# Kernel optimization log

Measured on AMD Instinct MI355X. Metric: run time of the kernel, lower is better.

Reference implementation:

```python
import jax, jax.numpy as jnp
import numpy as np

B, S, H, N_HEAD = 2, 2048, 1024, 16
NEG = float(-(2 ** 32) + 1)  # -4294967295.0, the module's padding value
EPS = 1e-08


def setup_inputs() -> dict:
    key = jax.random.key(0)
    ks = jax.random.split(key, 11)
    sc = 0.02
    return {
        "queries": jax.random.normal(ks[0], (B, S, H), dtype=jnp.float32),
        "keys": jax.random.normal(ks[1], (B, S, H), dtype=jnp.float32),
        "values": jax.random.normal(ks[2], (B, S, H), dtype=jnp.float32),
        "Wq": jax.random.normal(ks[3], (H, H), dtype=jnp.float32) * sc,
        "bq": jax.random.normal(ks[4], (H,), dtype=jnp.float32) * sc,
        "Wk": jax.random.normal(ks[5], (H, H), dtype=jnp.float32) * sc,
        "bk": jax.random.normal(ks[6], (H,), dtype=jnp.float32) * sc,
        "Wv": jax.random.normal(ks[7], (H, H), dtype=jnp.float32) * sc,
        "bv": jax.random.normal(ks[8], (H,), dtype=jnp.float32) * sc,
        "Wo": jax.random.normal(ks[9], (H, H), dtype=jnp.float32) * sc,
        "bo": jax.random.normal(ks[10], (H,), dtype=jnp.float32) * sc,
    }


def reference(queries, keys, values, Wq, bq, Wk, bk, Wv, bv, Wo, bo):
    n = N_HEAD
    Bb, Sq, Hh = queries.shape
    Sk = keys.shape[1]
    d = Hh // n

    # Linear + ReLU projections
    Q = jax.nn.relu(queries @ Wq + bq)  # [B,Sq,H]
    K = jax.nn.relu(keys @ Wk + bk)     # [B,Sk,H]
    V = jax.nn.relu(values @ Wv + bv)   # [B,Sk,H]

    # chunk(dim=2) + cat(dim=0) == head-major split: [n,B,S,d]
    Q_ = Q.reshape(Bb, Sq, n, d).transpose(2, 0, 1, 3)
    K_ = K.reshape(Bb, Sk, n, d).transpose(2, 0, 1, 3)
    V_ = V.reshape(Bb, Sk, n, d).transpose(2, 0, 1, 3)

    # key padding mask from full (pre-chunk) K: [B,Sk]
    key_masks = jnp.sign(jnp.abs(jnp.sum(K, axis=-1)))

    # scores: [n,B,Sq,Sk], scaled by sqrt(per-head dim)
    scores = jnp.einsum("hbqd,hbkd->hbqk", Q_, K_) / (d ** 0.5)

    # multiplicative padding-mask selection -> equivalent where()
    scores = jnp.where(key_masks[None, :, None, :] == 0.0, NEG, scores)

    # causal tril mask (masked=True)
    tril = jnp.tril(jnp.ones((Sq, Sk), dtype=scores.dtype))
    scores = jnp.where(tril[None, None] == 0.0, NEG, scores)

    attn = jax.nn.softmax(scores, axis=-1)
    out = jnp.einsum("hbqk,hbkd->hbqd", attn, V_)  # [n,B,Sq,d]

    # cat chunks back along feature dim: [B,Sq,H]
    out = out.transpose(1, 2, 0, 3).reshape(Bb, Sq, Hh)

    out = jax.nn.relu(out @ Wo + bo)
    # sublayer connection (dropout treated as identity for determinism)
    out = queries + out

    # layer norm with torch-style unbiased std, gamma=1, beta=0
    mean = out.mean(axis=-1, keepdims=True)
    std = jnp.std(out, axis=-1, ddof=1, keepdims=True)
    return (out - mean) / (std + EPS)
```

## Files before the change

### kernel.cpp

```cpp
#include <hip/hip_runtime.h>
#include <math.h>

typedef __bf16 bf16;
typedef __attribute__((ext_vector_type(8))) __bf16 bf16x8;
typedef __attribute__((ext_vector_type(4))) __bf16 bf16x4;
typedef __attribute__((ext_vector_type(4))) float f32x4;

typedef __attribute__((address_space(1))) unsigned int glb_u32;
typedef __attribute__((address_space(3))) unsigned int lds_u32;

#define NEGV (-4294967295.0f)
#define SCL2 0.18033688011112042f

__device__ __forceinline__ void async_cp16(const void* g, void* l) {
  __builtin_amdgcn_global_load_lds((glb_u32*)g, (lds_u32*)l, 16, 0, 0);
}

template <int CTRL>
__device__ __forceinline__ float dppf(float x) {
  return __builtin_bit_cast(float,
      __builtin_amdgcn_mov_dpp(__builtin_bit_cast(int, x), CTRL, 0xF, 0xF, true));
}
__device__ __forceinline__ float dpp_max16(float x) {
  x = fmaxf(x, dppf<0xB1>(x));
  x = fmaxf(x, dppf<0x4E>(x));
  x = fmaxf(x, dppf<0x141>(x));
  x = fmaxf(x, dppf<0x140>(x));
  return x;
}
__device__ __forceinline__ float dpp_sum16(float x) {
  x += dppf<0xB1>(x);
  x += dppf<0x4E>(x);
  x += dppf<0x141>(x);
  x += dppf<0x140>(x);
  return x;
}

__global__ __launch_bounds__(256) void cvt3_kernel(
    const float* __restrict__ q, const float* __restrict__ k,
    const float* __restrict__ v, short* xq, short* xk, short* xv) {
  const int bid = blockIdx.x;
  const int which = bid >> 12;
  const int i = (bid & 4095) * 256 + threadIdx.x;
  const float* src = which == 0 ? q : (which == 1 ? k : v);
  short* dst = which == 0 ? xq : (which == 1 ? xk : xv);
  float4 vv = ((const float4*)src)[i];
  bf16x4 o;
  o[0] = (bf16)vv.x; o[1] = (bf16)vv.y; o[2] = (bf16)vv.z; o[3] = (bf16)vv.w;
  ((bf16x4*)dst)[i] = o;
}

__global__ __launch_bounds__(256) void wt_kernel(
    const float* __restrict__ W0, const float* __restrict__ W1,
    const float* __restrict__ W2, const float* __restrict__ W3,
    short* T0, short* T1, short* T2, short* T3) {
  __shared__ float tile[64][65];
  const float* W = blockIdx.z == 0 ? W0 : (blockIdx.z == 1 ? W1 : (blockIdx.z == 2 ? W2 : W3));
  bf16* T = (bf16*)(blockIdx.z == 0 ? T0 : (blockIdx.z == 1 ? T1 : (blockIdx.z == 2 ? T2 : T3)));
  const int k0 = blockIdx.y * 64, n0 = blockIdx.x * 64;
  const int tid = threadIdx.x;
  const int c = tid & 63, rr = tid >> 6;
#pragma unroll
  for (int i = 0; i < 16; i++) {
    int r = i * 4 + rr;
    tile[r][c] = W[(size_t)(k0 + r) * 1024 + n0 + c];
  }
  __syncthreads();
#pragma unroll
  for (int i = 0; i < 16; i++) {
    int r = i * 4 + rr;
    T[(size_t)(n0 + r) * 1024 + k0 + c] = (bf16)tile[c][r];
  }
}

__global__ __launch_bounds__(256) void qkv_gemm(
    const short* Xq_, const short* Xk_, const short* Xv_,
    const short* Wtq_, const short* Wtk_, const short* Wtv_,
    const float* __restrict__ bq_, const float* __restrict__ bk_, const float* __restrict__ bv_,
    short* Qo_, short* Ko_, short* Vto_) {
  __shared__ bf16 Alds[128][32];
  __shared__ bf16 Blds[128][32];
  const int which = blockIdx.z;
  const bf16* X  = (const bf16*)(which == 0 ? Xq_  : (which == 1 ? Xk_  : Xv_));
  const bf16* Wt = (const bf16*)(which == 0 ? Wtq_ : (which == 1 ? Wtk_ : Wtv_));
  const float* bias = which == 0 ? bq_ : (which == 1 ? bk_ : bv_);
  const int m0 = blockIdx.y * 128, n0 = blockIdx.x * 128;
  const int tid = threadIdx.x, wid = tid >> 6, lane = tid & 63;
  const int wr = wid >> 1, wc = wid & 1;
  const int l15 = lane & 15, lg = lane >> 4;
  const f32x4 vzero = {0.f, 0.f, 0.f, 0.f};
  f32x4 acc[4][4];
#pragma unroll
  for (int m = 0; m < 4; m++)
#pragma unroll
    for (int n = 0; n < 4; n++) acc[m][n] = vzero;

  const int sr = wid * 32 + (lane >> 2);
  const int scb = (lane & 3) * 16;

  for (int kt = 0; kt < 32; ++kt) {
    const char* ga = (const char*)(X + (size_t)(m0 + sr) * 1024 + kt * 32) + scb;
    async_cp16(ga, &Alds[wid * 32][0]);
    async_cp16(ga + 16 * 2048, &Alds[wid * 32 + 16][0]);
    const char* gb = (const char*)(Wt + (size_t)(n0 + sr) * 1024 + kt * 32) + scb;
    async_cp16(gb, &Blds[wid * 32][0]);
    async_cp16(gb + 16 * 2048, &Blds[wid * 32 + 16][0]);
    __syncthreads();
    bf16x8 a[4], bb[4];
#pragma unroll
    for (int m = 0; m < 4; m++) a[m] = *(const bf16x8*)&Alds[wr * 64 + m * 16 + l15][lg * 8];
#pragma unroll
    for (int n = 0; n < 4; n++) bb[n] = *(const bf16x8*)&Blds[wc * 64 + n * 16 + l15][lg * 8];
#pragma unroll
    for (int m = 0; m < 4; m++)
#pragma unroll
      for (int n = 0; n < 4; n++)
        acc[m][n] = __builtin_amdgcn_mfma_f32_16x16x32_bf16(a[m], bb[n], acc[m][n], 0, 0, 0);
    __syncthreads();
  }

  if (which != 2) {
    bf16* Y = (bf16*)(which == 0 ? Qo_ : Ko_);
    const float osc = (which == 0) ? SCL2 : 1.0f;
#pragma unroll
    for (int n = 0; n < 4; n++) {
      const int col = n0 + wc * 64 + n * 16 + l15;
      const float bv = bias[col];
#pragma unroll
      for (int m = 0; m < 4; m++) {
        const int row0 = m0 + wr * 64 + m * 16 + lg * 4;
#pragma unroll
        for (int r = 0; r < 4; r++) {
          float v = acc[m][n][r] + bv;
          v = v > 0.f ? v : 0.f;
          Y[(size_t)(row0 + r) * 1024 + col] = (bf16)(v * osc);
        }
      }
    }
  } else {
    bf16* Vt = (bf16*)Vto_;
#pragma unroll
    for (int n = 0; n < 4; n++) {
      const int col = n0 + wc * 64 + n * 16 + l15;
      const float bv = bias[col];
#pragma unroll
      for (int m = 0; m < 4; m++) {
        const int row0 = m0 + wr * 64 + m * 16 + lg * 4;
        const int bb2 = row0 >> 11;
        const int s = row0 & 2047;
        bf16x4 pk;
#pragma unroll
        for (int r = 0; r < 4; r++) {
          float v = acc[m][n][r] + bv;
          v = v > 0.f ? v : 0.f;
          pk[r] = (bf16)v;
        }
        *(bf16x4*)(Vt + ((size_t)bb2 * 1024 + col) * 2048 + s) = pk;
      }
    }
  }
}

__global__ __launch_bounds__(256) void out_gemm(
    const short* A_, const short* Wt_, const float* __restrict__ bias,
    float* __restrict__ Y) {
  __shared__ bf16 Alds[128][32];
  __shared__ bf16 Blds[128][32];
  const bf16* X = (const bf16*)A_;
  const bf16* Wt = (const bf16*)Wt_;
  const int m0 = blockIdx.y * 128, n0 = blockIdx.x * 128;
  const int tid = threadIdx.x, wid = tid >> 6, lane = tid & 63;
  const int wr = wid >> 1, wc = wid & 1;
  const int l15 = lane & 15, lg = lane >> 4;
  const f32x4 vzero = {0.f, 0.f, 0.f, 0.f};
  f32x4 acc[4][4];
#pragma unroll
  for (int m = 0; m < 4; m++)
#pragma unroll
    for (int n = 0; n < 4; n++) acc[m][n] = vzero;

  const int sr = wid * 32 + (lane >> 2);
  const int scb = (lane & 3) * 16;

  for (int kt = 0; kt < 32; ++kt) {
    const char* ga = (const char*)(X + (size_t)(m0 + sr) * 1024 + kt * 32) + scb;
    async_cp16(ga, &Alds[wid * 32][0]);
    async_cp16(ga + 16 * 2048, &Alds[wid * 32 + 16][0]);
    const char* gb = (const char*)(Wt + (size_t)(n0 + sr) * 1024 + kt * 32) + scb;
    async_cp16(gb, &Blds[wid * 32][0]);
    async_cp16(gb + 16 * 2048, &Blds[wid * 32 + 16][0]);
    __syncthreads();
    bf16x8 a[4], bb[4];
#pragma unroll
    for (int m = 0; m < 4; m++) a[m] = *(const bf16x8*)&Alds[wr * 64 + m * 16 + l15][lg * 8];
#pragma unroll
    for (int n = 0; n < 4; n++) bb[n] = *(const bf16x8*)&Blds[wc * 64 + n * 16 + l15][lg * 8];
#pragma unroll
    for (int m = 0; m < 4; m++)
#pragma unroll
      for (int n = 0; n < 4; n++)
        acc[m][n] = __builtin_amdgcn_mfma_f32_16x16x32_bf16(a[m], bb[n], acc[m][n], 0, 0, 0);
    __syncthreads();
  }
#pragma unroll
  for (int n = 0; n < 4; n++) {
    const int col = n0 + wc * 64 + n * 16 + l15;
    const float bv = bias[col];
#pragma unroll
    for (int m = 0; m < 4; m++) {
      const int row0 = m0 + wr * 64 + m * 16 + lg * 4;
#pragma unroll
      for (int r = 0; r < 4; r++) {
        float v = acc[m][n][r] + bv;
        Y[(size_t)(row0 + r) * 1024 + col] = v > 0.f ? v : 0.f;
      }
    }
  }
}

__global__ __launch_bounds__(256) void key_mask_kernel(const short* Kb_,
                                                       float* __restrict__ mask) {
  const bf16* Kb = (const bf16*)Kb_;
  const int row = blockIdx.x * 4 + (threadIdx.x >> 6);
  const int lane = threadIdx.x & 63;
  const bf16x8* p = (const bf16x8*)(Kb + (size_t)row * 1024);
  float s = 0.f;
#pragma unroll
  for (int i = 0; i < 2; i++) {
    bf16x8 v = p[i * 64 + lane];
#pragma unroll
    for (int j = 0; j < 8; j++) s += (float)v[j];
  }
  for (int m = 32; m; m >>= 1) s += __shfl_xor(s, m);
  if (lane == 0) mask[row] = (s != 0.f) ? 1.f : 0.f;
}

__device__ __forceinline__ bf16x8 lds_read_swz(const bf16* base, int row, int cbyte) {
  return *(const bf16x8*)((const char*)base + row * 128 + (cbyte ^ ((row & 7) << 4)));
}

__global__ __launch_bounds__(128) void attn_kernel(
    const short* Q_, const short* K_, const short* Vt_,
    const float* __restrict__ kmask, short* O_) {
  __shared__ bf16 Klds[2][64][64];
  __shared__ bf16 Vlds[2][64][64];
  __shared__ bf16 Plds[2][16][64];
  const bf16* Q = (const bf16*)Q_;
  const bf16* K = (const bf16*)K_;
  const bf16* Vt = (const bf16*)Vt_;
  bf16* O = (bf16*)O_;

  const int f = blockIdx.x;
  const int xcd = f & 7, idx = f >> 3;
  const int qtb = idx & 31;
  const int hb = xcd + 8 * (idx >> 5);
  const int h = hb & 15, b = hb >> 4;

  const int tid = threadIdx.x, wid = tid >> 6, lane = tid & 63;
  const int l15 = lane & 15, lg = lane >> 4;
  const f32x4 vzero = {0.f, 0.f, 0.f, 0.f};
  bf16* const pbase = &Plds[wid][0][0];

  const int srow = lane >> 3;
  const int cb = (lane & 7) * 16;
  const int cbs = cb ^ ((srow & 7) << 4);

  for (int seg = 0; seg < 2; ++seg) {
    const int qt = (seg == 0) ? qtb : 63 - qtb;
    const int q0 = qt * 32;
    const int nkt = (32 * qt + 95) >> 6;

    const int qrow = q0 + wid * 16 + l15;
    const bf16* qp = Q + ((size_t)b * 2048 + qrow) * 1024 + h * 64;
    const bf16x8 qf0 = *(const bf16x8*)(qp + lg * 8);
    const bf16x8 qf1 = *(const bf16x8*)(qp + 32 + lg * 8);

    float Mrow[4], Lrow[4];
    f32x4 oacc[4];
#pragma unroll
    for (int r = 0; r < 4; r++) { Mrow[r] = -INFINITY; Lrow[r] = 0.f; }
#pragma unroll
    for (int n = 0; n < 4; n++) oacc[n] = vzero;

    auto STAGE = [&](int buf, int kt) {
#pragma unroll
      for (int c = 0; c < 4; c++) {
        const int r = wid * 32 + c * 8 + srow;
        const char* gk = (const char*)(K + ((size_t)b * 2048 + kt * 64 + r) * 1024 + h * 64);
        async_cp16(gk + cbs, &Klds[buf][wid * 32 + c * 8][0]);
        const char* gv = (const char*)(Vt + ((size_t)b * 1024 + h * 64 + r) * 2048 + kt * 64);
        async_cp16(gv + cbs, &Vlds[buf][wid * 32 + c * 8][0]);
      }
    };

    STAGE(0, 0);
    __syncthreads();
    int cur = 0;
    for (int kt = 0; kt < nkt; ++kt) {
      if (kt + 1 < nkt) STAGE(cur ^ 1, kt + 1);

      f32x4 sacc[4];
#pragma unroll
      for (int n = 0; n < 4; n++) sacc[n] = vzero;
      {
        bf16x8 kf[4];
#pragma unroll
        for (int n = 0; n < 4; n++)
          kf[n] = lds_read_swz(&Klds[cur][0][0], n * 16 + l15, lg * 16);
        __builtin_amdgcn_s_setprio(1);
#pragma unroll
        for (int n = 0; n < 4; n++)
          sacc[n] = __builtin_amdgcn_mfma_f32_16x16x32_bf16(qf0, kf[n], sacc[n], 0, 0, 0);
        __builtin_amdgcn_s_setprio(0);
#pragma unroll
        for (int n = 0; n < 4; n++)
          kf[n] = lds_read_swz(&Klds[cur][0][0], n * 16 + l15, 64 + lg * 16);
        __builtin_amdgcn_s_setprio(1);
#pragma unroll
        for (int n = 0; n < 4; n++)
          sacc[n] = __builtin_amdgcn_mfma_f32_16x16x32_bf16(qf1, kf[n], sacc[n], 0, 0, 0);
        __builtin_amdgcn_s_setprio(0);
      }

      const int qrow0 = q0 + wid * 16 + lg * 4;
      const bool last = (kt == nkt - 1);
#pragma unroll
      for (int n = 0; n < 4; n++) {
        const int kcol = kt * 64 + n * 16 + l15;
        const float kmv = kmask[b * 2048 + kcol];
        const bool mz = (kmv == 0.f);
#pragma unroll
        for (int r = 0; r < 4; r++) {
          float sc = sacc[n][r];
          if (mz) sc = NEGV;
          if (last && kcol > qrow0 + r) sc = NEGV;
          sacc[n][r] = sc;
        }
      }

      {
        float tm[4];
#pragma unroll
        for (int r = 0; r < 4; r++) {
          float t = fmaxf(fmaxf(sacc[0][r], sacc[1][r]), fmaxf(sacc[2][r], sacc[3][r]));
          tm[r] = dpp_max16(t);
        }
        const int defer = __all((tm[0] - Mrow[0] <= 8.f) & (tm[1] - Mrow[1] <= 8.f) &
                                (tm[2] - Mrow[2] <= 8.f) & (tm[3] - Mrow[3] <= 8.f));
        if (!defer) {
#pragma unroll
          for (int r = 0; r < 4; r++) {
            const float Mn = fmaxf(Mrow[r], tm[r]);
            const float sc = exp2f(Mrow[r] - Mn);
            Mrow[r] = Mn;
            Lrow[r] *= sc;
#pragma unroll
            for (int n = 0; n < 4; n++) oacc[n][r] *= sc;
          }
        }
        float rs[4] = {0.f, 0.f, 0.f, 0.f};
#pragma unroll
        for (int n = 0; n < 4; n++)
#pragma unroll
          for (int r = 0; r < 4; r++) {
            const float p = exp2f(sacc[n][r] - Mrow[r]);
            rs[r] += p;
            const int prow = lg * 4 + r;
            *(bf16*)((char*)pbase + prow * 128 +
                     (((n * 16 + l15) * 2) ^ ((prow & 7) << 4))) = (bf16)p;
          }
#pragma unroll
        for (int r = 0; r < 4; r++) Lrow[r] += dpp_sum16(rs[r]);
      }

#pragma unroll
      for (int ks = 0; ks < 2; ks++) {
        bf16x8 vf[4];
#pragma unroll
        for (int nd = 0; nd < 4; nd++)
          vf[nd] = lds_read_swz(&Vlds[cur][0][0], nd * 16 + l15, ks * 64 + lg * 16);
        const bf16x8 pf = lds_read_swz(pbase, l15, ks * 64 + lg * 16);
        __builtin_amdgcn_s_setprio(1);
#pragma unroll
        for (int nd = 0; nd < 4; nd++)
          oacc[nd] = __builtin_amdgcn_mfma_f32_16x16x32_bf16(pf, vf[nd], oacc[nd], 0, 0, 0);
        __builtin_amdgcn_s_setprio(0);
      }

      __syncthreads();
      cur ^= 1;
    }

    float inv[4];
#pragma unroll
    for (int r = 0; r < 4; r++) inv[r] = 1.0f / Lrow[r];
#pragma unroll
    for (int nd = 0; nd < 4; nd++) {
      const int col = h * 64 + nd * 16 + l15;
#pragma unroll
      for (int r = 0; r < 4; r++) {
        const float v = oacc[nd][r] * inv[r];
        O[((size_t)b * 2048 + q0 + wid * 16 + lg * 4 + r) * 1024 + col] = (bf16)v;
      }
    }
  }
}

__global__ __launch_bounds__(256) void ln_kernel(const float* __restrict__ qin,
                                                 const float* __restrict__ proj,
                                                 float* __restrict__ out) {
  __shared__ float sbuf[4];
  const int row = blockIdx.x, tid = threadIdx.x;
  const size_t base = (size_t)row * 1024 + tid * 4;
  const float4 a = *(const float4*)(qin + base);
  const float4 p = *(const float4*)(proj + base);
  const float x0 = a.x + p.x, x1 = a.y + p.y, x2 = a.z + p.z, x3 = a.w + p.w;
  float s = x0 + x1 + x2 + x3;
  for (int m = 32; m; m >>= 1) s += __shfl_xor(s, m);
  if ((tid & 63) == 0) sbuf[tid >> 6] = s;
  __syncthreads();
  s = sbuf[0] + sbuf[1] + sbuf[2] + sbuf[3];
  const float mean = s * (1.f / 1024.f);
  const float d0 = x0 - mean, d1 = x1 - mean, d2 = x2 - mean, d3 = x3 - mean;
  float ss = d0 * d0 + d1 * d1 + d2 * d2 + d3 * d3;
  __syncthreads();
  for (int m = 32; m; m >>= 1) ss += __shfl_xor(ss, m);
  if ((tid & 63) == 0) sbuf[tid >> 6] = ss;
  __syncthreads();
  ss = sbuf[0] + sbuf[1] + sbuf[2] + sbuf[3];
  const float inv = 1.f / (sqrtf(ss * (1.f / 1023.f)) + 1e-8f);
  float4 o;
  o.x = d0 * inv; o.y = d1 * inv; o.z = d2 * inv; o.w = d3 * inv;
  *(float4*)(out + base) = o;
}

extern "C" void kernel_launch(void* const* d_in, const int* in_sizes, int n_in,
                              void* d_out, int out_size, void* d_ws, size_t ws_size,
                              hipStream_t stream) {
  (void)in_sizes; (void)n_in; (void)out_size; (void)ws_size;
  const float* queries = (const float*)d_in[0];
  const float* keys    = (const float*)d_in[1];
  const float* values  = (const float*)d_in[2];
  const float* Wq = (const float*)d_in[3];  const float* bq = (const float*)d_in[4];
  const float* Wk = (const float*)d_in[5];  const float* bk = (const float*)d_in[6];
  const float* Wv = (const float*)d_in[7];  const float* bv = (const float*)d_in[8];
  const float* Wo = (const float*)d_in[9];  const float* bo = (const float*)d_in[10];
  float* out = (float*)d_out;

  char* w = (char*)d_ws;
  const size_t SZ_X = (size_t)4096 * 1024 * 2;
  const size_t SZ_W = (size_t)1024 * 1024 * 2;
  short* Xq  = (short*)w; w += SZ_X;
  short* Xk  = (short*)w; w += SZ_X;
  short* Xv  = (short*)w; w += SZ_X;
  short* Wtq = (short*)w; w += SZ_W;
  short* Wtk = (short*)w; w += SZ_W;
  short* Wtv = (short*)w; w += SZ_W;
  short* Wto = (short*)w; w += SZ_W;
  short* Qb  = (short*)w; w += SZ_X;
  short* Kb  = (short*)w; w += SZ_X;
  short* Vtb = (short*)w; w += SZ_X;
  short* Ab  = (short*)w; w += SZ_X;
  float* km  = (float*)w; w += (size_t)4096 * sizeof(float);
  float* proj = (float*)w; w += (size_t)4096 * 1024 * 4;

  cvt3_kernel<<<12288, 256, 0, stream>>>(queries, keys, values, Xq, Xk, Xv);
  wt_kernel<<<dim3(16, 16, 4), 256, 0, stream>>>(Wq, Wk, Wv, Wo, Wtq, Wtk, Wtv, Wto);
  qkv_gemm<<<dim3(8, 32, 3), 256, 0, stream>>>(Xq, Xk, Xv, Wtq, Wtk, Wtv,
                                               bq, bk, bv, Qb, Kb, Vtb);
  key_mask_kernel<<<1024, 256, 0, stream>>>(Kb, km);
  attn_kernel<<<1024, 128, 0, stream>>>(Qb, Kb, Vtb, km, Ab);
  out_gemm<<<dim3(8, 32), 256, 0, stream>>>(Ab, Wto, bo, proj);
  ln_kernel<<<4096, 256, 0, stream>>>(queries, proj, out);
}
```

Measured before the change: 168.3 us.

## Restructure attention into single-wave blocks with 32-key tiles and bitmask key mask

Attention now runs as 2048 single-wave blocks, each handling a 32-row query tile over 32-key tiles, with a new block ordering that balances causal work. The old version used two-wave blocks that each processed a paired short and long query tile. Because a block is one wave, __syncthreads is gone and the copy pipeline waits on explicit vmcnt counts. The key padding mask is packed into 32-bit words by a smaller kernel, and the softmax row sum is computed by an MFMA against a ones vector instead of DPP reductions. Smaller tiles mean more loop iterations and more per-tile overhead.

```diff
diff --git a/kernel.cpp b/kernel.cpp
--- a/kernel.cpp
+++ b/kernel.cpp
@@ -26,13 +26,6 @@
   x = fmaxf(x, dppf<0x4E>(x));
   x = fmaxf(x, dppf<0x141>(x));
   x = fmaxf(x, dppf<0x140>(x));
-  return x;
-}
-__device__ __forceinline__ float dpp_sum16(float x) {
-  x += dppf<0xB1>(x);
-  x += dppf<0x4E>(x);
-  x += dppf<0x141>(x);
-  x += dppf<0x140>(x);
   return x;
 }
 
@@ -219,32 +212,41 @@
 }
 
 __global__ __launch_bounds__(256) void key_mask_kernel(const short* Kb_,
-                                                       float* __restrict__ mask) {
+                                                       unsigned* __restrict__ kbits) {
+  __shared__ unsigned bits[4];
   const bf16* Kb = (const bf16*)Kb_;
-  const int row = blockIdx.x * 4 + (threadIdx.x >> 6);
-  const int lane = threadIdx.x & 63;
-  const bf16x8* p = (const bf16x8*)(Kb + (size_t)row * 1024);
-  float s = 0.f;
-#pragma unroll
-  for (int i = 0; i < 2; i++) {
-    bf16x8 v = p[i * 64 + lane];
-#pragma unroll
-    for (int j = 0; j < 8; j++) s += (float)v[j];
-  }
-  for (int m = 32; m; m >>= 1) s += __shfl_xor(s, m);
-  if (lane == 0) mask[row] = (s != 0.f) ? 1.f : 0.f;
-}
-
-__device__ __forceinline__ bf16x8 lds_read_swz(const bf16* base, int row, int cbyte) {
-  return *(const bf16x8*)((const char*)base + row * 128 + (cbyte ^ ((row & 7) << 4)));
-}
-
-__global__ __launch_bounds__(128) void attn_kernel(
+  const int wid = threadIdx.x >> 6, lane = threadIdx.x & 63;
+  const int row0 = blockIdx.x * 32 + wid * 8;
+  unsigned mybits = 0;
+#pragma unroll
+  for (int i = 0; i < 8; i++) {
+    const bf16x8* p = (const bf16x8*)(Kb + (size_t)(row0 + i) * 1024);
+    bf16x8 v0 = p[lane];
+    bf16x8 v1 = p[64 + lane];
+    float s = 0.f;
+#pragma unroll
+    for (int jj = 0; jj < 8; jj++) s += (float)v0[jj] + (float)v1[jj];
+    for (int m = 32; m; m >>= 1) s += __shfl_xor(s, m);
+    if (s != 0.f) mybits |= 1u << (wid * 8 + i);
+  }
+  if (lane == 0) bits[wid] = mybits;
+  __syncthreads();
+  if (threadIdx.x == 0) kbits[blockIdx.x] = bits[0] | bits[1] | bits[2] | bits[3];
+}
+
+__device__ __forceinline__ bf16x8 ldsK(const bf16* base, int row, int cb) {
+  return *(const bf16x8*)((const char*)base + row * 128 + (cb ^ ((row & 7) << 4)));
+}
+__device__ __forceinline__ bf16x8 lds64(const bf16* base, int row, int cb) {
+  return *(const bf16x8*)((const char*)base + row * 64 + (cb ^ (((row >> 1) & 3) << 4)));
+}
+
+__global__ __launch_bounds__(64) void attn_kernel(
     const short* Q_, const short* K_, const short* Vt_,
-    const float* __restrict__ kmask, short* O_) {
-  __shared__ bf16 Klds[2][64][64];
-  __shared__ bf16 Vlds[2][64][64];
-  __shared__ bf16 Plds[2][16][64];
+    const unsigned* __restrict__ kbits, short* O_) {
+  __shared__ bf16 Klds[2][32][64];
+  __shared__ bf16 Vlds[2][64][32];
+  __shared__ bf16 Plds[32][32];
   const bf16* Q = (const bf16*)Q_;
   const bf16* K = (const bf16*)K_;
   const bf16* Vt = (const bf16*)Vt_;
@@ -252,155 +254,189 @@
 
   const int f = blockIdx.x;
   const int xcd = f & 7, idx = f >> 3;
-  const int qtb = idx & 31;
-  const int hb = xcd + 8 * (idx >> 5);
+  const int hbp = idx >> 6, j = idx & 63;
+  const int jj = j & 31;
+  const int tb = (jj & 1) ? 63 - jj : jj;
+  const int t = (j & 32) ? 63 - tb : tb;
+  const int hb = xcd + 8 * hbp;
   const int h = hb & 15, b = hb >> 4;
-
-  const int tid = threadIdx.x, wid = tid >> 6, lane = tid & 63;
+  const int q0 = t * 32, nkt = t + 1;
+
+  const int lane = threadIdx.x;
   const int l15 = lane & 15, lg = lane >> 4;
   const f32x4 vzero = {0.f, 0.f, 0.f, 0.f};
-  bf16* const pbase = &Plds[wid][0][0];
-
-  const int srow = lane >> 3;
-  const int cb = (lane & 7) * 16;
-  const int cbs = cb ^ ((srow & 7) << 4);
-
-  for (int seg = 0; seg < 2; ++seg) {
-    const int qt = (seg == 0) ? qtb : 63 - qtb;
-    const int q0 = qt * 32;
-    const int nkt = (32 * qt + 95) >> 6;
-
-    const int qrow = q0 + wid * 16 + l15;
-    const bf16* qp = Q + ((size_t)b * 2048 + qrow) * 1024 + h * 64;
-    const bf16x8 qf0 = *(const bf16x8*)(qp + lg * 8);
-    const bf16x8 qf1 = *(const bf16x8*)(qp + 32 + lg * 8);
-
-    float Mrow[4], Lrow[4];
-    f32x4 oacc[4];
-#pragma unroll
-    for (int r = 0; r < 4; r++) { Mrow[r] = -INFINITY; Lrow[r] = 0.f; }
-#pragma unroll
-    for (int n = 0; n < 4; n++) oacc[n] = vzero;
-
-    auto STAGE = [&](int buf, int kt) {
-#pragma unroll
-      for (int c = 0; c < 4; c++) {
-        const int r = wid * 32 + c * 8 + srow;
-        const char* gk = (const char*)(K + ((size_t)b * 2048 + kt * 64 + r) * 1024 + h * 64);
-        async_cp16(gk + cbs, &Klds[buf][wid * 32 + c * 8][0]);
-        const char* gv = (const char*)(Vt + ((size_t)b * 1024 + h * 64 + r) * 2048 + kt * 64);
-        async_cp16(gv + cbs, &Vlds[buf][wid * 32 + c * 8][0]);
-      }
-    };
-
-    STAGE(0, 0);
-    __syncthreads();
-    int cur = 0;
-    for (int kt = 0; kt < nkt; ++kt) {
-      if (kt + 1 < nkt) STAGE(cur ^ 1, kt + 1);
-
-      f32x4 sacc[4];
-#pragma unroll
-      for (int n = 0; n < 4; n++) sacc[n] = vzero;
-      {
-        bf16x8 kf[4];
-#pragma unroll
-        for (int n = 0; n < 4; n++)
-          kf[n] = lds_read_swz(&Klds[cur][0][0], n * 16 + l15, lg * 16);
-        __builtin_amdgcn_s_setprio(1);
-#pragma unroll
-        for (int n = 0; n < 4; n++)
-          sacc[n] = __builtin_amdgcn_mfma_f32_16x16x32_bf16(qf0, kf[n], sacc[n], 0, 0, 0);
-        __builtin_amdgcn_s_setprio(0);
-#pragma unroll
-        for (int n = 0; n < 4; n++)
-          kf[n] = lds_read_swz(&Klds[cur][0][0], n * 16 + l15, 64 + lg * 16);
-        __builtin_amdgcn_s_setprio(1);
-#pragma unroll
-        for (int n = 0; n < 4; n++)
-          sacc[n] = __builtin_amdgcn_mfma_f32_16x16x32_bf16(qf1, kf[n], sacc[n], 0, 0, 0);
-        __builtin_amdgcn_s_setprio(0);
-      }
-
-      const int qrow0 = q0 + wid * 16 + lg * 4;
-      const bool last = (kt == nkt - 1);
-#pragma unroll
-      for (int n = 0; n < 4; n++) {
-        const int kcol = kt * 64 + n * 16 + l15;
-        const float kmv = kmask[b * 2048 + kcol];
-        const bool mz = (kmv == 0.f);
+
+  const int ksrow = lane >> 3;
+  const int kcb = ((lane & 7) * 16) ^ (ksrow << 4);
+  const int vsrow = lane >> 2;
+  const int vcb = ((lane & 3) * 16) ^ (((vsrow >> 1) & 3) << 4);
+
+  bf16x8 qf[2][2];
+#pragma unroll
+  for (int m = 0; m < 2; m++) {
+    const bf16* qp = Q + ((size_t)b * 2048 + q0 + m * 16 + l15) * 1024 + h * 64;
+#pragma unroll
+    for (int ks = 0; ks < 2; ks++) qf[m][ks] = *(const bf16x8*)(qp + ks * 32 + lg * 8);
+  }
+
+  bf16x8 vones;
+#pragma unroll
+  for (int i = 0; i < 8; i++) vones[i] = (bf16)1.0f;
+
+  float Mrow[2][4];
+  f32x4 oacc[2][4], oaccL[2];
+#pragma unroll
+  for (int m = 0; m < 2; m++) {
+#pragma unroll
+    for (int r = 0; r < 4; r++) Mrow[m][r] = -INFINITY;
+#pragma unroll
+    for (int nd = 0; nd < 4; nd++) oacc[m][nd] = vzero;
+    oaccL[m] = vzero;
+  }
+  float Mmin = -INFINITY;
+
+  auto STAGE = [&](int buf, int kt) {
+#pragma unroll
+    for (int c = 0; c < 4; c++) {
+      const char* gk = (const char*)(K + ((size_t)b * 2048 + kt * 32 + c * 8 + ksrow) * 1024 + h * 64) + kcb;
+      async_cp16(gk, &Klds[buf][c * 8][0]);
+    }
+#pragma unroll
+    for (int c = 0; c < 4; c++) {
+      const char* gv = (const char*)(Vt + ((size_t)b * 1024 + h * 64 + c * 16 + vsrow) * 2048 + kt * 32) + vcb;
+      async_cp16(gv, &Vlds[buf][c * 16][0]);
+    }
+  };
+
+  STAGE(0, 0);
+  int cur = 0;
+  for (int kt = 0; kt < nkt; ++kt) {
+    if (kt + 1 < nkt) {
+      STAGE(cur ^ 1, kt + 1);
+      asm volatile("s_waitcnt vmcnt(8)" ::: "memory");
+    } else {
+      asm volatile("s_waitcnt vmcnt(0)" ::: "memory");
+    }
+    __builtin_amdgcn_sched_barrier(0);
+
+    f32x4 sacc[2][2];
+#pragma unroll
+    for (int m = 0; m < 2; m++)
+#pragma unroll
+      for (int n = 0; n < 2; n++) sacc[m][n] = vzero;
+#pragma unroll
+    for (int ks = 0; ks < 2; ks++) {
+      bf16x8 kf0 = ldsK(&Klds[cur][0][0], l15, ks * 64 + lg * 16);
+      bf16x8 kf1 = ldsK(&Klds[cur][0][0], 16 + l15, ks * 64 + lg * 16);
+      __builtin_amdgcn_s_setprio(1);
+#pragma unroll
+      for (int m = 0; m < 2; m++) {
+        sacc[m][0] = __builtin_amdgcn_mfma_f32_16x16x32_bf16(qf[m][ks], kf0, sacc[m][0], 0, 0, 0);
+        sacc[m][1] = __builtin_amdgcn_mfma_f32_16x16x32_bf16(qf[m][ks], kf1, sacc[m][1], 0, 0, 0);
+      }
+      __builtin_amdgcn_s_setprio(0);
+    }
+
+    const unsigned wb = kbits[(b << 6) + kt];
+#pragma unroll
+    for (int n = 0; n < 2; n++) {
+      const bool on = (wb >> (n * 16 + l15)) & 1;
+      if (!on) {
+#pragma unroll
+        for (int m = 0; m < 2; m++)
+#pragma unroll
+          for (int r = 0; r < 4; r++) sacc[m][n][r] = NEGV;
+      }
+    }
+    if (kt == nkt - 1) {
+#pragma unroll
+      for (int m = 0; m < 2; m++)
+#pragma unroll
+        for (int n = 0; n < 2; n++) {
+          const int c16 = n * 16 + l15;
+#pragma unroll
+          for (int r = 0; r < 4; r++)
+            if (c16 > m * 16 + lg * 4 + r) sacc[m][n][r] = NEGV;
+        }
+    }
+
+    {
+      float lm = sacc[0][0][0];
+#pragma unroll
+      for (int m = 0; m < 2; m++)
+#pragma unroll
+        for (int n = 0; n < 2; n++)
+#pragma unroll
+          for (int r = 0; r < 4; r++) lm = fmaxf(lm, sacc[m][n][r]);
+      const float gmax = dpp_max16(lm);
+      if (!__all(gmax <= Mmin + 8.f)) {
+#pragma unroll
+        for (int m = 0; m < 2; m++)
+#pragma unroll
+          for (int r = 0; r < 4; r++) {
+            float tm = fmaxf(sacc[m][0][r], sacc[m][1][r]);
+            tm = dpp_max16(tm);
+            const float Mn = fmaxf(Mrow[m][r], tm);
+            const float sc = exp2f(Mrow[m][r] - Mn);
+            Mrow[m][r] = Mn;
+#pragma unroll
+            for (int nd = 0; nd < 4; nd++) oacc[m][nd][r] *= sc;
+            oaccL[m][r] *= sc;
+          }
+        float mm = Mrow[0][0];
+#pragma unroll
+        for (int m = 0; m < 2; m++)
+#pragma unroll
+          for (int r = 0; r < 4; r++) mm = fminf(mm, Mrow[m][r]);
+        Mmin = mm;
+      }
+    }
+
+#pragma unroll
+    for (int m = 0; m < 2; m++)
+#pragma unroll
+      for (int n = 0; n < 2; n++)
 #pragma unroll
         for (int r = 0; r < 4; r++) {
-          float sc = sacc[n][r];
-          if (mz) sc = NEGV;
-          if (last && kcol > qrow0 + r) sc = NEGV;
-          sacc[n][r] = sc;
+          const float p = exp2f(sacc[m][n][r] - Mrow[m][r]);
+          const int prow = m * 16 + lg * 4 + r;
+          *(bf16*)((char*)&Plds[0][0] + prow * 64 +
+                   (((n * 16 + l15) * 2) ^ (((prow >> 1) & 3) << 4))) = (bf16)p;
         }
-      }
-
-      {
-        float tm[4];
-#pragma unroll
-        for (int r = 0; r < 4; r++) {
-          float t = fmaxf(fmaxf(sacc[0][r], sacc[1][r]), fmaxf(sacc[2][r], sacc[3][r]));
-          tm[r] = dpp_max16(t);
-        }
-        const int defer = __all((tm[0] - Mrow[0] <= 8.f) & (tm[1] - Mrow[1] <= 8.f) &
-                                (tm[2] - Mrow[2] <= 8.f) & (tm[3] - Mrow[3] <= 8.f));
-        if (!defer) {
-#pragma unroll
-          for (int r = 0; r < 4; r++) {
-            const float Mn = fmaxf(Mrow[r], tm[r]);
-            const float sc = exp2f(Mrow[r] - Mn);
-            Mrow[r] = Mn;
-            Lrow[r] *= sc;
-#pragma unroll
-            for (int n = 0; n < 4; n++) oacc[n][r] *= sc;
-          }
-        }
-        float rs[4] = {0.f, 0.f, 0.f, 0.f};
-#pragma unroll
-        for (int n = 0; n < 4; n++)
-#pragma unroll
-          for (int r = 0; r < 4; r++) {
-            const float p = exp2f(sacc[n][r] - Mrow[r]);
-            rs[r] += p;
-            const int prow = lg * 4 + r;
-            *(bf16*)((char*)pbase + prow * 128 +
-                     (((n * 16 + l15) * 2) ^ ((prow & 7) << 4))) = (bf16)p;
-          }
-#pragma unroll
-        for (int r = 0; r < 4; r++) Lrow[r] += dpp_sum16(rs[r]);
-      }
-
-#pragma unroll
-      for (int ks = 0; ks < 2; ks++) {
-        bf16x8 vf[4];
-#pragma unroll
-        for (int nd = 0; nd < 4; nd++)
-          vf[nd] = lds_read_swz(&Vlds[cur][0][0], nd * 16 + l15, ks * 64 + lg * 16);
-        const bf16x8 pf = lds_read_swz(pbase, l15, ks * 64 + lg * 16);
-        __builtin_amdgcn_s_setprio(1);
-#pragma unroll
-        for (int nd = 0; nd < 4; nd++)
-          oacc[nd] = __builtin_amdgcn_mfma_f32_16x16x32_bf16(pf, vf[nd], oacc[nd], 0, 0, 0);
-        __builtin_amdgcn_s_setprio(0);
-      }
-
-      __syncthreads();
-      cur ^= 1;
-    }
-
+
+    {
+      bf16x8 pf0 = lds64(&Plds[0][0], l15, lg * 16);
+      bf16x8 pf1 = lds64(&Plds[0][0], 16 + l15, lg * 16);
+      bf16x8 vf[4];
+#pragma unroll
+      for (int nd = 0; nd < 4; nd++)
+        vf[nd] = lds64(&Vlds[cur][0][0], nd * 16 + l15, lg * 16);
+      __builtin_amdgcn_s_setprio(1);
+#pragma unroll
+      for (int nd = 0; nd < 4; nd++) {
+        oacc[0][nd] = __builtin_amdgcn_mfma_f32_16x16x32_bf16(pf0, vf[nd], oacc[0][nd], 0, 0, 0);
+        oacc[1][nd] = __builtin_amdgcn_mfma_f32_16x16x32_bf16(pf1, vf[nd], oacc[1][nd], 0, 0, 0);
+      }
+      oaccL[0] = __builtin_amdgcn_mfma_f32_16x16x32_bf16(pf0, vones, oaccL[0], 0, 0, 0);
+      oaccL[1] = __builtin_amdgcn_mfma_f32_16x16x32_bf16(pf1, vones, oaccL[1], 0, 0, 0);
+      __builtin_amdgcn_s_setprio(0);
+    }
+
+    cur ^= 1;
+  }
+
+#pragma unroll
+  for (int m = 0; m < 2; m++) {
     float inv[4];
 #pragma unroll
-    for (int r = 0; r < 4; r++) inv[r] = 1.0f / Lrow[r];
+    for (int r = 0; r < 4; r++) inv[r] = 1.0f / oaccL[m][r];
 #pragma unroll
     for (int nd = 0; nd < 4; nd++) {
       const int col = h * 64 + nd * 16 + l15;
 #pragma unroll
       for (int r = 0; r < 4; r++) {
-        const float v = oacc[nd][r] * inv[r];
-        O[((size_t)b * 2048 + q0 + wid * 16 + lg * 4 + r) * 1024 + col] = (bf16)v;
+        const float v = oacc[m][nd][r] * inv[r];
+        O[((size_t)b * 2048 + q0 + m * 16 + lg * 4 + r) * 1024 + col] = (bf16)v;
       }
     }
   }
@@ -461,15 +497,15 @@
   short* Kb  = (short*)w; w += SZ_X;
   short* Vtb = (short*)w; w += SZ_X;
   short* Ab  = (short*)w; w += SZ_X;
-  float* km  = (float*)w; w += (size_t)4096 * sizeof(float);
+  unsigned* kbits = (unsigned*)w; w += 4096;
   float* proj = (float*)w; w += (size_t)4096 * 1024 * 4;
 
   cvt3_kernel<<<12288, 256, 0, stream>>>(queries, keys, values, Xq, Xk, Xv);
   wt_kernel<<<dim3(16, 16, 4), 256, 0, stream>>>(Wq, Wk, Wv, Wo, Wtq, Wtk, Wtv, Wto);
   qkv_gemm<<<dim3(8, 32, 3), 256, 0, stream>>>(Xq, Xk, Xv, Wtq, Wtk, Wtv,
                                                bq, bk, bv, Qb, Kb, Vtb);
-  key_mask_kernel<<<1024, 256, 0, stream>>>(Kb, km);
-  attn_kernel<<<1024, 128, 0, stream>>>(Qb, Kb, Vtb, km, Ab);
+  key_mask_kernel<<<128, 256, 0, stream>>>(Kb, kbits);
+  attn_kernel<<<2048, 64, 0, stream>>>(Qb, Kb, Vtb, kbits, Ab);
   out_gemm<<<dim3(8, 32), 256, 0, stream>>>(Ab, Wto, bo, proj);
   ln_kernel<<<4096, 256, 0, stream>>>(queries, proj, out);
 }
```

After: 181.8 us. +8.0%, slower.

## Compute softmax row sums via MFMA, bit-pack key mask, coarsen max deferral check

Applied to the files above, without the earlier changes.

The softmax denominator is now accumulated by an extra MFMA of P against a vector of ones, which removes the per-row DPP sum reductions. The key padding mask is packed into 32-bit words, so the attention kernel does two scalar loads per tile instead of per-lane float loads. The lazy-rescale test now compares a single combined max against the smallest running max and only computes per-row maxima when a rescale is needed. In exchange there is one extra MFMA per k-step, the denominator is summed from bf16-rounded probabilities, and the mask kernel runs with fewer, larger blocks.

```diff
diff --git a/kernel.cpp b/kernel.cpp
--- a/kernel.cpp
+++ b/kernel.cpp
@@ -26,13 +26,6 @@
   x = fmaxf(x, dppf<0x4E>(x));
   x = fmaxf(x, dppf<0x141>(x));
   x = fmaxf(x, dppf<0x140>(x));
-  return x;
-}
-__device__ __forceinline__ float dpp_sum16(float x) {
-  x += dppf<0xB1>(x);
-  x += dppf<0x4E>(x);
-  x += dppf<0x141>(x);
-  x += dppf<0x140>(x);
   return x;
 }
 
@@ -219,20 +212,26 @@
 }
 
 __global__ __launch_bounds__(256) void key_mask_kernel(const short* Kb_,
-                                                       float* __restrict__ mask) {
+                                                       unsigned* __restrict__ kbits) {
+  __shared__ unsigned bits[4];
   const bf16* Kb = (const bf16*)Kb_;
-  const int row = blockIdx.x * 4 + (threadIdx.x >> 6);
-  const int lane = threadIdx.x & 63;
-  const bf16x8* p = (const bf16x8*)(Kb + (size_t)row * 1024);
-  float s = 0.f;
-#pragma unroll
-  for (int i = 0; i < 2; i++) {
-    bf16x8 v = p[i * 64 + lane];
-#pragma unroll
-    for (int j = 0; j < 8; j++) s += (float)v[j];
-  }
-  for (int m = 32; m; m >>= 1) s += __shfl_xor(s, m);
-  if (lane == 0) mask[row] = (s != 0.f) ? 1.f : 0.f;
+  const int wid = threadIdx.x >> 6, lane = threadIdx.x & 63;
+  const int row0 = blockIdx.x * 32 + wid * 8;
+  unsigned mybits = 0;
+#pragma unroll
+  for (int i = 0; i < 8; i++) {
+    const bf16x8* p = (const bf16x8*)(Kb + (size_t)(row0 + i) * 1024);
+    bf16x8 v0 = p[lane];
+    bf16x8 v1 = p[64 + lane];
+    float s = 0.f;
+#pragma unroll
+    for (int jj = 0; jj < 8; jj++) s += (float)v0[jj] + (float)v1[jj];
+    for (int m = 32; m; m >>= 1) s += __shfl_xor(s, m);
+    if (s != 0.f) mybits |= 1u << (wid * 8 + i);
+  }
+  if (lane == 0) bits[wid] = mybits;
+  __syncthreads();
+  if (threadIdx.x == 0) kbits[blockIdx.x] = bits[0] | bits[1] | bits[2] | bits[3];
 }
 
 __device__ __forceinline__ bf16x8 lds_read_swz(const bf16* base, int row, int cbyte) {
@@ -241,7 +240,7 @@
 
 __global__ __launch_bounds__(128) void attn_kernel(
     const short* Q_, const short* K_, const short* Vt_,
-    const float* __restrict__ kmask, short* O_) {
+    const unsigned* __restrict__ kbits, short* O_) {
   __shared__ bf16 Klds[2][64][64];
   __shared__ bf16 Vlds[2][64][64];
   __shared__ bf16 Plds[2][16][64];
@@ -265,6 +264,10 @@
   const int cb = (lane & 7) * 16;
   const int cbs = cb ^ ((srow & 7) << 4);
 
+  bf16x8 vones;
+#pragma unroll
+  for (int i = 0; i < 8; i++) vones[i] = (bf16)1.0f;
+
   for (int seg = 0; seg < 2; ++seg) {
     const int qt = (seg == 0) ? qtb : 63 - qtb;
     const int q0 = qt * 32;
@@ -275,12 +278,14 @@
     const bf16x8 qf0 = *(const bf16x8*)(qp + lg * 8);
     const bf16x8 qf1 = *(const bf16x8*)(qp + 32 + lg * 8);
 
-    float Mrow[4], Lrow[4];
-    f32x4 oacc[4];
-#pragma unroll
-    for (int r = 0; r < 4; r++) { Mrow[r] = -INFINITY; Lrow[r] = 0.f; }
+    float Mrow[4];
+    f32x4 oacc[4], oaccL;
+#pragma unroll
+    for (int r = 0; r < 4; r++) Mrow[r] = -INFINITY;
 #pragma unroll
     for (int n = 0; n < 4; n++) oacc[n] = vzero;
+    oaccL = vzero;
+    float Mmin = -INFINITY;
 
     auto STAGE = [&](int buf, int kt) {
 #pragma unroll
@@ -322,56 +327,56 @@
         __builtin_amdgcn_s_setprio(0);
       }
 
+      const unsigned w0 = kbits[b * 64 + kt * 2];
+      const unsigned w1 = kbits[b * 64 + kt * 2 + 1];
       const int qrow0 = q0 + wid * 16 + lg * 4;
       const bool last = (kt == nkt - 1);
 #pragma unroll
       for (int n = 0; n < 4; n++) {
+        const unsigned wsel = (n < 2) ? w0 : w1;
+        const bool on = (wsel >> ((n & 1) * 16 + l15)) & 1;
         const int kcol = kt * 64 + n * 16 + l15;
-        const float kmv = kmask[b * 2048 + kcol];
-        const bool mz = (kmv == 0.f);
 #pragma unroll
         for (int r = 0; r < 4; r++) {
           float sc = sacc[n][r];
-          if (mz) sc = NEGV;
+          if (!on) sc = NEGV;
           if (last && kcol > qrow0 + r) sc = NEGV;
           sacc[n][r] = sc;
         }
       }
 
       {
-        float tm[4];
-#pragma unroll
-        for (int r = 0; r < 4; r++) {
-          float t = fmaxf(fmaxf(sacc[0][r], sacc[1][r]), fmaxf(sacc[2][r], sacc[3][r]));
-          tm[r] = dpp_max16(t);
-        }
-        const int defer = __all((tm[0] - Mrow[0] <= 8.f) & (tm[1] - Mrow[1] <= 8.f) &
-                                (tm[2] - Mrow[2] <= 8.f) & (tm[3] - Mrow[3] <= 8.f));
-        if (!defer) {
+        float lm = sacc[0][0];
+#pragma unroll
+        for (int n = 0; n < 4; n++)
+#pragma unroll
+          for (int r = 0; r < 4; r++) lm = fmaxf(lm, sacc[n][r]);
+        const float gmax = dpp_max16(lm);
+        if (!__all(gmax <= Mmin + 8.f)) {
 #pragma unroll
           for (int r = 0; r < 4; r++) {
-            const float Mn = fmaxf(Mrow[r], tm[r]);
+            float tm = fmaxf(fmaxf(sacc[0][r], sacc[1][r]), fmaxf(sacc[2][r], sacc[3][r]));
+            tm = dpp_max16(tm);
+            const float Mn = fmaxf(Mrow[r], tm);
             const float sc = exp2f(Mrow[r] - Mn);
             Mrow[r] = Mn;
-            Lrow[r] *= sc;
 #pragma unroll
             for (int n = 0; n < 4; n++) oacc[n][r] *= sc;
+            oaccL[r] *= sc;
           }
+          Mmin = fminf(fminf(Mrow[0], Mrow[1]), fminf(Mrow[2], Mrow[3]));
         }
-        float rs[4] = {0.f, 0.f, 0.f, 0.f};
-#pragma unroll
-        for (int n = 0; n < 4; n++)
-#pragma unroll
-          for (int r = 0; r < 4; r++) {
-            const float p = exp2f(sacc[n][r] - Mrow[r]);
-            rs[r] += p;
-            const int prow = lg * 4 + r;
-            *(bf16*)((char*)pbase + prow * 128 +
-                     (((n * 16 + l15) * 2) ^ ((prow & 7) << 4))) = (bf16)p;
-          }
-#pragma unroll
-        for (int r = 0; r < 4; r++) Lrow[r] += dpp_sum16(rs[r]);
-      }
+      }
+
+#pragma unroll
+      for (int n = 0; n < 4; n++)
+#pragma unroll
+        for (int r = 0; r < 4; r++) {
+          const float p = exp2f(sacc[n][r] - Mrow[r]);
+          const int prow = lg * 4 + r;
+          *(bf16*)((char*)pbase + prow * 128 +
+                   (((n * 16 + l15) * 2) ^ ((prow & 7) << 4))) = (bf16)p;
+        }
 
 #pragma unroll
       for (int ks = 0; ks < 2; ks++) {
@@ -384,6 +389,7 @@
 #pragma unroll
         for (int nd = 0; nd < 4; nd++)
           oacc[nd] = __builtin_amdgcn_mfma_f32_16x16x32_bf16(pf, vf[nd], oacc[nd], 0, 0, 0);
+        oaccL = __builtin_amdgcn_mfma_f32_16x16x32_bf16(pf, vones, oaccL, 0, 0, 0);
         __builtin_amdgcn_s_setprio(0);
       }
 
@@ -393,7 +399,7 @@
 
     float inv[4];
 #pragma unroll
-    for (int r = 0; r < 4; r++) inv[r] = 1.0f / Lrow[r];
+    for (int r = 0; r < 4; r++) inv[r] = 1.0f / oaccL[r];
 #pragma unroll
     for (int nd = 0; nd < 4; nd++) {
       const int col = h * 64 + nd * 16 + l15;
@@ -461,15 +467,15 @@
   short* Kb  = (short*)w; w += SZ_X;
   short* Vtb = (short*)w; w += SZ_X;
   short* Ab  = (short*)w; w += SZ_X;
-  float* km  = (float*)w; w += (size_t)4096 * sizeof(float);
+  unsigned* kbits = (unsigned*)w; w += 4096;
   float* proj = (float*)w; w += (size_t)4096 * 1024 * 4;
 
   cvt3_kernel<<<12288, 256, 0, stream>>>(queries, keys, values, Xq, Xk, Xv);
   wt_kernel<<<dim3(16, 16, 4), 256, 0, stream>>>(Wq, Wk, Wv, Wo, Wtq, Wtk, Wtv, Wto);
   qkv_gemm<<<dim3(8, 32, 3), 256, 0, stream>>>(Xq, Xk, Xv, Wtq, Wtk, Wtv,
                                                bq, bk, bv, Qb, Kb, Vtb);
-  key_mask_kernel<<<1024, 256, 0, stream>>>(Kb, km);
-  attn_kernel<<<1024, 128, 0, stream>>>(Qb, Kb, Vtb, km, Ab);
+  key_mask_kernel<<<128, 256, 0, stream>>>(Kb, kbits);
+  attn_kernel<<<1024, 128, 0, stream>>>(Qb, Kb, Vtb, kbits, Ab);
   out_gemm<<<dim3(8, 32), 256, 0, stream>>>(Ab, Wto, bo, proj);
   ln_kernel<<<4096, 256, 0, stream>>>(queries, proj, out);
 }
```

After: 158.5 us. -5.8%, faster.
